# Kernel optimization log

Measured on AMD Instinct MI355X. Metric: run time of the kernel, lower is better.

Reference implementation:

```python
import jax, jax.numpy as jnp
import numpy as np

B = 4096       # batch size
DIM = 1024     # feature dim
E = 9          # 8 session experts + 1 default layer (index 8)


def setup_inputs() -> dict:
    key = jax.random.key(0)
    k_x, k_w, k_b, k_i = jax.random.split(key, 4)
    x = jax.random.normal(k_x, (B, DIM), dtype=jnp.float32)
    # Stacked nn.Linear params: W[e] has torch layout [out, in], b[e] is [out].
    # (Original init is identity+zero bias; random values exercise the same math.)
    W = jax.random.normal(k_w, (E, DIM, DIM), dtype=jnp.float32) * (DIM ** -0.5)
    b = jax.random.normal(k_b, (E, DIM), dtype=jnp.float32)
    session_idx = jax.random.randint(k_i, (B,), 0, E, dtype=jnp.int64)
    return {"x": x, "W": W, "b": b, "session_idx": session_idx}


def reference(x, W, b, session_idx):
    # Per-sample keyed linear: out[i] = x[i] @ W[session_idx[i]].T + b[session_idx[i]].
    # Dense formulation: run every expert on every sample (E small), then select.
    # y: [B, E, DIM]
    y = jnp.einsum('bd,eod->beo', x, W) + b[None, :, :]
    out = y[jnp.arange(x.shape[0]), session_idx]  # [B, DIM]
    return out
```

## Files before the change

### kernel.cpp

```cpp
#include <hip/hip_runtime.h>
#include <hip/hip_bf16.h>

#define NE 9
#define NDIM 1024
#define BM 64
#define BN 128
#define BK 64
#define NT (NDIM / BK)
#define MAX_SLOTS 80

typedef __attribute__((ext_vector_type(8))) short bf16x8;
typedef __attribute__((ext_vector_type(4))) float f32x4;

__device__ __forceinline__ unsigned pack2_bf16(float a, float b) {
    __hip_bfloat162 h = __float22bfloat162_rn(float2{a, b});
    return *reinterpret_cast<unsigned*>(&h);
}

__global__ __launch_bounds__(512)
void bucket_kernel(const int* __restrict__ sidx,
                   int* __restrict__ perm,
                   int* __restrict__ offsets,
                   int* __restrict__ slot_e,
                   int* __restrict__ slot_m0,
                   int* __restrict__ nslots,
                   int nB) {
    __shared__ int cnt[NE];
    __shared__ int cur[NE];
    int t = threadIdx.x;
    if (t < NE) cnt[t] = 0;
    __syncthreads();
    for (int i = t; i < nB; i += 512) atomicAdd(&cnt[sidx[i]], 1);
    __syncthreads();
    if (t == 0) {
        int run = 0, s = 0;
        for (int e = 0; e < NE; ++e) {
            cur[e] = run; offsets[e] = run;
            for (int m0 = 0; m0 < cnt[e]; m0 += BM) {
                slot_e[s] = e; slot_m0[s] = m0; ++s;
            }
            run += cnt[e];
        }
        offsets[NE] = run;
        *nslots = s;
    }
    __syncthreads();
    for (int i = t; i < nB; i += 512) {
        int p = atomicAdd(&cur[sidx[i]], 1);
        perm[p] = i;
    }
}

__global__ __launch_bounds__(256, 3)
void gemm_fused_kernel(const float* __restrict__ x,
                       const float* __restrict__ W,
                       const float* __restrict__ bias,
                       const int* __restrict__ perm,
                       const int* __restrict__ offsets,
                       const int* __restrict__ slot_e,
                       const int* __restrict__ slot_m0,
                       const int* __restrict__ nslots,
                       float* __restrict__ out) {
    const int b    = blockIdx.x;
    const int xcd  = b & 7;
    const int j    = b >> 3;
    const int ns   = *nslots;
    const int q    = ns >> 3, r = ns & 7;
    const int mine = q + (xcd < r ? 1 : 0);
    const int ls   = j >> 3;
    if (ls >= mine) return;
    const int slot = xcd * q + (xcd < r ? xcd : r) + ls;
    const int n    = j & 7;

    const int e   = slot_e[slot];
    const int m0  = slot_m0[slot];
    const int off = offsets[e];
    const int cnt = offsets[e + 1] - off;
    const int n0  = n * BN;

    __shared__ __align__(16) unsigned short lds[24576];

    const int t    = threadIdx.x;
    const int wave = t >> 6;
    const int lane = t & 63;
    const int fr   = lane & 15;
    const int fq   = lane >> 4;
    const int wr   = (wave >> 1) * 32;
    const int wc   = (wave & 1) * 64;
    const int xr   = fr & 7;

    const int c8 = t & 7;
    const int rg = t >> 3;
    const int wcol = (c8 ^ (rg & 7)) * 8;

    int ar0 = m0 + rg;      if (ar0 >= cnt) ar0 = cnt - 1;
    int ar1 = m0 + 32 + rg; if (ar1 >= cnt) ar1 = cnt - 1;
    const float* ap0 = x + (size_t)perm[off + ar0] * NDIM + c8 * 8;
    const float* ap1 = x + (size_t)perm[off + ar1] * NDIM + c8 * 8;
    const float* bp  = W + ((size_t)e * NDIM + n0 + rg) * NDIM + c8 * 8;

    float4 sa[4], sb[8];

#define LOADR(K0)                                                              \
    do {                                                                       \
        sa[0] = *(const float4*)(ap0 + (K0));                                  \
        sa[1] = *(const float4*)(ap0 + (K0) + 4);                              \
        sa[2] = *(const float4*)(ap1 + (K0));                                  \
        sa[3] = *(const float4*)(ap1 + (K0) + 4);                              \
        sb[0] = *(const float4*)(bp + (K0));                                   \
        sb[1] = *(const float4*)(bp + (K0) + 4);                               \
        sb[2] = *(const float4*)(bp + (size_t)32 * NDIM + (K0));               \
        sb[3] = *(const float4*)(bp + (size_t)32 * NDIM + (K0) + 4);           \
        sb[4] = *(const float4*)(bp + (size_t)64 * NDIM + (K0));               \
        sb[5] = *(const float4*)(bp + (size_t)64 * NDIM + (K0) + 4);           \
        sb[6] = *(const float4*)(bp + (size_t)96 * NDIM + (K0));               \
        sb[7] = *(const float4*)(bp + (size_t)96 * NDIM + (K0) + 4);           \
    } while (0)

#define PKW(DST, U, V)                                                         \
    do {                                                                       \
        uint4 o;                                                               \
        o.x = pack2_bf16((U).x, (U).y);                                        \
        o.y = pack2_bf16((U).z, (U).w);                                        \
        o.z = pack2_bf16((V).x, (V).y);                                        \
        o.w = pack2_bf16((V).z, (V).w);                                        \
        *reinterpret_cast<uint4*>(DST) = o;                                    \
    } while (0)

#define CVTW(BUF)                                                              \
    do {                                                                       \
        PKW(&lds[(BUF) * 4096 + rg * 64 + wcol], sa[0], sa[1]);                \
        PKW(&lds[(BUF) * 4096 + (32 + rg) * 64 + wcol], sa[2], sa[3]);         \
        PKW(&lds[8192 + (BUF) * 8192 + rg * 64 + wcol], sb[0], sb[1]);         \
        PKW(&lds[8192 + (BUF) * 8192 + (32 + rg) * 64 + wcol], sb[2], sb[3]);  \
        PKW(&lds[8192 + (BUF) * 8192 + (64 + rg) * 64 + wcol], sb[4], sb[5]);  \
        PKW(&lds[8192 + (BUF) * 8192 + (96 + rg) * 64 + wcol], sb[6], sb[7]);  \
    } while (0)

    f32x4 acc[2][4];
#pragma unroll
    for (int i = 0; i < 2; ++i)
#pragma unroll
        for (int k = 0; k < 4; ++k) acc[i][k] = (f32x4)(0.0f);

    LOADR(0);
    CVTW(0);
    LOADR(BK);
    __syncthreads();

    for (int tt = 0; tt < NT; ++tt) {
        const int curb = tt & 1;

#pragma unroll
        for (int kk = 0; kk < 2; ++kk) {
            const int cs = ((kk * 4 + fq) ^ xr) * 8;
            bf16x8 af[2], bfv[4];
#pragma unroll
            for (int mf = 0; mf < 2; ++mf)
                af[mf] = *reinterpret_cast<const bf16x8*>(
                    &lds[curb * 4096 + (wr + mf * 16 + fr) * 64 + cs]);
#pragma unroll
            for (int nf = 0; nf < 4; ++nf)
                bfv[nf] = *reinterpret_cast<const bf16x8*>(
                    &lds[8192 + curb * 8192 + (wc + nf * 16 + fr) * 64 + cs]);
            __builtin_amdgcn_s_setprio(1);
#pragma unroll
            for (int mf = 0; mf < 2; ++mf)
#pragma unroll
                for (int nf = 0; nf < 4; ++nf)
                    acc[mf][nf] = __builtin_amdgcn_mfma_f32_16x16x32_bf16(
                        af[mf], bfv[nf], acc[mf][nf], 0, 0, 0);
            __builtin_amdgcn_s_setprio(0);
        }

        if (tt + 1 < NT) {
            CVTW(curb ^ 1);
            if (tt + 2 < NT) LOADR((tt + 2) * BK);
            __syncthreads();
        }
    }
#undef LOADR
#undef PKW
#undef CVTW

    float bl[4];
#pragma unroll
    for (int nf = 0; nf < 4; ++nf)
        bl[nf] = bias[e * NDIM + n0 + wc + nf * 16 + fr];

#pragma unroll
    for (int mf = 0; mf < 2; ++mf) {
#pragma unroll
        for (int jr = 0; jr < 4; ++jr) {
            int lm = wr + mf * 16 + fq * 4 + jr;
            if (m0 + lm < cnt) {
                int grow = perm[off + m0 + lm];
                float* orow = out + (size_t)grow * NDIM;
#pragma unroll
                for (int nf = 0; nf < 4; ++nf)
                    orow[n0 + wc + nf * 16 + fr] = acc[mf][nf][jr] + bl[nf];
            }
        }
    }
}

extern "C" void kernel_launch(void* const* d_in, const int* in_sizes, int n_in,
                              void* d_out, int out_size, void* d_ws, size_t ws_size,
                              hipStream_t stream) {
    const float* x    = (const float*)d_in[0];
    const float* W    = (const float*)d_in[1];
    const float* bias = (const float*)d_in[2];
    const int*   sidx = (const int*)d_in[3];
    float*       out  = (float*)d_out;

    const int nB = in_sizes[3];

    char* wsb = (char*)d_ws;
    int* perm    = (int*)wsb;
    int* offsets = (int*)(wsb + (size_t)nB * 4);
    int* slot_e  = offsets + NE + 1;
    int* slot_m0 = slot_e + MAX_SLOTS;
    int* nslots  = slot_m0 + MAX_SLOTS;

    bucket_kernel<<<1, 512, 0, stream>>>(sidx, perm, offsets, slot_e, slot_m0,
                                         nslots, nB);

    gemm_fused_kernel<<<MAX_SLOTS * 8, 256, 0, stream>>>(
        x, W, bias, perm, offsets, slot_e, slot_m0, nslots, out);
}
```

Before: 45.19 us.

## Pre-convert x and W to bf16 and stream tiles via direct global-to-LDS loads

A prep kernel now converts all of x and W to bf16 in workspace while block 0 does the bucketing. The GEMM then loads bf16 tiles straight into LDS with global_load_lds, using a three-stage buffer and vmcnt waits instead of register staging and in-loop conversion. The aim is to halve GEMM load traffic and take conversion work off the main loop, at the cost of a full extra read and write pass over W and x. A naive fallback kernel runs if the workspace is too small.

```diff
diff --git a/kernel.cpp b/kernel.cpp
--- a/kernel.cpp
+++ b/kernel.cpp
@@ -17,50 +17,81 @@
     return *reinterpret_cast<unsigned*>(&h);
 }
 
-__global__ __launch_bounds__(512)
-void bucket_kernel(const int* __restrict__ sidx,
-                   int* __restrict__ perm,
-                   int* __restrict__ offsets,
-                   int* __restrict__ slot_e,
-                   int* __restrict__ slot_m0,
-                   int* __restrict__ nslots,
-                   int nB) {
-    __shared__ int cnt[NE];
-    __shared__ int cur[NE];
-    int t = threadIdx.x;
-    if (t < NE) cnt[t] = 0;
-    __syncthreads();
-    for (int i = t; i < nB; i += 512) atomicAdd(&cnt[sidx[i]], 1);
-    __syncthreads();
-    if (t == 0) {
-        int run = 0, s = 0;
-        for (int e = 0; e < NE; ++e) {
-            cur[e] = run; offsets[e] = run;
-            for (int m0 = 0; m0 < cnt[e]; m0 += BM) {
-                slot_e[s] = e; slot_m0[s] = m0; ++s;
+__device__ __forceinline__ void gload_lds16(const void* g, void* l) {
+    __builtin_amdgcn_global_load_lds(
+        (const __attribute__((address_space(1))) unsigned int*)g,
+        (__attribute__((address_space(3))) unsigned int*)l, 16, 0, 0);
+}
+
+__global__ __launch_bounds__(256)
+void prep_kernel(const float* __restrict__ x, const float* __restrict__ W,
+                 const int* __restrict__ sidx,
+                 unsigned short* __restrict__ xb, unsigned short* __restrict__ Wb,
+                 int* __restrict__ perm, int* __restrict__ offsets,
+                 int* __restrict__ slot_e, int* __restrict__ slot_m0,
+                 int* __restrict__ nslots, int nB) {
+    if (blockIdx.x == 0) {
+        __shared__ int cnt[NE];
+        __shared__ int cur[NE];
+        int t = threadIdx.x;
+        if (t < NE) cnt[t] = 0;
+        __syncthreads();
+        for (int i = t; i < nB; i += 256) atomicAdd(&cnt[sidx[i]], 1);
+        __syncthreads();
+        if (t == 0) {
+            int run = 0, s = 0;
+            for (int e = 0; e < NE; ++e) {
+                cur[e] = run; offsets[e] = run;
+                for (int m0 = 0; m0 < cnt[e]; m0 += BM) {
+                    slot_e[s] = e; slot_m0[s] = m0; ++s;
+                }
+                run += cnt[e];
             }
-            run += cnt[e];
-        }
-        offsets[NE] = run;
-        *nslots = s;
-    }
-    __syncthreads();
-    for (int i = t; i < nB; i += 512) {
-        int p = atomicAdd(&cur[sidx[i]], 1);
-        perm[p] = i;
-    }
-}
-
-__global__ __launch_bounds__(256, 3)
-void gemm_fused_kernel(const float* __restrict__ x,
-                       const float* __restrict__ W,
-                       const float* __restrict__ bias,
-                       const int* __restrict__ perm,
-                       const int* __restrict__ offsets,
-                       const int* __restrict__ slot_e,
-                       const int* __restrict__ slot_m0,
-                       const int* __restrict__ nslots,
-                       float* __restrict__ out) {
+            offsets[NE] = run;
+            *nslots = s;
+        }
+        __syncthreads();
+        for (int i = t; i < nB; i += 256) {
+            int p = atomicAdd(&cur[sidx[i]], 1);
+            perm[p] = i;
+        }
+    } else {
+        const int NW8 = NE * NDIM * (NDIM / 8);
+        const int NX8 = nB * (NDIM / 8);
+        const int tot = NW8 + NX8;
+        const int stride = (gridDim.x - 1) * 256;
+        for (int u = (blockIdx.x - 1) * 256 + threadIdx.x; u < tot; u += stride) {
+            const float4* src;
+            uint4* dst;
+            if (u < NW8) {
+                src = (const float4*)W + 2 * (size_t)u;
+                dst = (uint4*)Wb + u;
+            } else {
+                size_t v = (size_t)(u - NW8);
+                src = (const float4*)x + 2 * v;
+                dst = (uint4*)xb + v;
+            }
+            float4 a = src[0], c = src[1];
+            uint4 o;
+            o.x = pack2_bf16(a.x, a.y);
+            o.y = pack2_bf16(a.z, a.w);
+            o.z = pack2_bf16(c.x, c.y);
+            o.w = pack2_bf16(c.z, c.w);
+            *dst = o;
+        }
+    }
+}
+
+__global__ __launch_bounds__(256, 2)
+void gemm_bf16_kernel(const unsigned short* __restrict__ xb,
+                      const unsigned short* __restrict__ Wb,
+                      const float* __restrict__ bias,
+                      const int* __restrict__ perm,
+                      const int* __restrict__ offsets,
+                      const int* __restrict__ slot_e,
+                      const int* __restrict__ slot_m0,
+                      const int* __restrict__ nslots,
+                      float* __restrict__ out) {
     const int b    = blockIdx.x;
     const int xcd  = b & 7;
     const int j    = b >> 3;
@@ -78,7 +109,7 @@
     const int cnt = offsets[e + 1] - off;
     const int n0  = n * BN;
 
-    __shared__ __align__(16) unsigned short lds[24576];
+    __shared__ __align__(16) unsigned short lds[36864];
 
     const int t    = threadIdx.x;
     const int wave = t >> 6;
@@ -89,68 +120,47 @@
     const int wc   = (wave & 1) * 64;
     const int xr   = fr & 7;
 
-    const int c8 = t & 7;
-    const int rg = t >> 3;
-    const int wcol = (c8 ^ (rg & 7)) * 8;
-
-    int ar0 = m0 + rg;      if (ar0 >= cnt) ar0 = cnt - 1;
-    int ar1 = m0 + 32 + rg; if (ar1 >= cnt) ar1 = cnt - 1;
-    const float* ap0 = x + (size_t)perm[off + ar0] * NDIM + c8 * 8;
-    const float* ap1 = x + (size_t)perm[off + ar1] * NDIM + c8 * 8;
-    const float* bp  = W + ((size_t)e * NDIM + n0 + rg) * NDIM + c8 * 8;
-
-    float4 sa[4], sb[8];
-
-#define LOADR(K0)                                                              \
+    const int srow = t >> 3;
+    const int scol = ((t & 7) ^ (srow & 7)) * 8;
+    int lm0 = m0 + srow;      if (lm0 >= cnt) lm0 = cnt - 1;
+    int lm1 = m0 + 32 + srow; if (lm1 >= cnt) lm1 = cnt - 1;
+    const unsigned short* asrc0 = xb + (size_t)perm[off + lm0] * NDIM + scol;
+    const unsigned short* asrc1 = xb + (size_t)perm[off + lm1] * NDIM + scol;
+    const unsigned short* bsrc  = Wb + ((size_t)e * NDIM + n0 + srow) * NDIM + scol;
+
+#define STAGE(BUF, K0)                                                         \
     do {                                                                       \
-        sa[0] = *(const float4*)(ap0 + (K0));                                  \
-        sa[1] = *(const float4*)(ap0 + (K0) + 4);                              \
-        sa[2] = *(const float4*)(ap1 + (K0));                                  \
-        sa[3] = *(const float4*)(ap1 + (K0) + 4);                              \
-        sb[0] = *(const float4*)(bp + (K0));                                   \
-        sb[1] = *(const float4*)(bp + (K0) + 4);                               \
-        sb[2] = *(const float4*)(bp + (size_t)32 * NDIM + (K0));               \
-        sb[3] = *(const float4*)(bp + (size_t)32 * NDIM + (K0) + 4);           \
-        sb[4] = *(const float4*)(bp + (size_t)64 * NDIM + (K0));               \
-        sb[5] = *(const float4*)(bp + (size_t)64 * NDIM + (K0) + 4);           \
-        sb[6] = *(const float4*)(bp + (size_t)96 * NDIM + (K0));               \
-        sb[7] = *(const float4*)(bp + (size_t)96 * NDIM + (K0) + 4);           \
+        const int _ab = (BUF) * 4096;                                          \
+        const int _bb = 12288 + (BUF) * 8192;                                  \
+        gload_lds16(asrc0 + (K0), &lds[_ab + wave * 512]);                     \
+        gload_lds16(asrc1 + (K0), &lds[_ab + 2048 + wave * 512]);              \
+        _Pragma("unroll")                                                      \
+        for (int i = 0; i < 4; ++i)                                            \
+            gload_lds16(bsrc + (size_t)i * 32 * NDIM + (K0),                   \
+                        &lds[_bb + i * 2048 + wave * 512]);                    \
     } while (0)
 
-#define PKW(DST, U, V)                                                         \
-    do {                                                                       \
-        uint4 o;                                                               \
-        o.x = pack2_bf16((U).x, (U).y);                                        \
-        o.y = pack2_bf16((U).z, (U).w);                                        \
-        o.z = pack2_bf16((V).x, (V).y);                                        \
-        o.w = pack2_bf16((V).z, (V).w);                                        \
-        *reinterpret_cast<uint4*>(DST) = o;                                    \
-    } while (0)
-
-#define CVTW(BUF)                                                              \
-    do {                                                                       \
-        PKW(&lds[(BUF) * 4096 + rg * 64 + wcol], sa[0], sa[1]);                \
-        PKW(&lds[(BUF) * 4096 + (32 + rg) * 64 + wcol], sa[2], sa[3]);         \
-        PKW(&lds[8192 + (BUF) * 8192 + rg * 64 + wcol], sb[0], sb[1]);         \
-        PKW(&lds[8192 + (BUF) * 8192 + (32 + rg) * 64 + wcol], sb[2], sb[3]);  \
-        PKW(&lds[8192 + (BUF) * 8192 + (64 + rg) * 64 + wcol], sb[4], sb[5]);  \
-        PKW(&lds[8192 + (BUF) * 8192 + (96 + rg) * 64 + wcol], sb[6], sb[7]);  \
-    } while (0)
-
     f32x4 acc[2][4];
 #pragma unroll
     for (int i = 0; i < 2; ++i)
 #pragma unroll
         for (int k = 0; k < 4; ++k) acc[i][k] = (f32x4)(0.0f);
 
-    LOADR(0);
-    CVTW(0);
-    LOADR(BK);
-    __syncthreads();
-
+    STAGE(0, 0);
+    STAGE(1, BK);
+    asm volatile("s_waitcnt vmcnt(6)" ::: "memory");
+    __builtin_amdgcn_s_barrier();
+
+    int cur = 0;
+#pragma unroll
     for (int tt = 0; tt < NT; ++tt) {
-        const int curb = tt & 1;
-
+        if (tt + 2 < NT) {
+            int sb = cur + 2; if (sb >= 3) sb -= 3;
+            STAGE(sb, (tt + 2) * BK);
+        }
+
+        const int abase = cur * 4096;
+        const int bbase = 12288 + cur * 8192;
 #pragma unroll
         for (int kk = 0; kk < 2; ++kk) {
             const int cs = ((kk * 4 + fq) ^ xr) * 8;
@@ -158,30 +168,29 @@
 #pragma unroll
             for (int mf = 0; mf < 2; ++mf)
                 af[mf] = *reinterpret_cast<const bf16x8*>(
-                    &lds[curb * 4096 + (wr + mf * 16 + fr) * 64 + cs]);
+                    &lds[abase + (wr + mf * 16 + fr) * 64 + cs]);
 #pragma unroll
             for (int nf = 0; nf < 4; ++nf)
                 bfv[nf] = *reinterpret_cast<const bf16x8*>(
-                    &lds[8192 + curb * 8192 + (wc + nf * 16 + fr) * 64 + cs]);
-            __builtin_amdgcn_s_setprio(1);
+                    &lds[bbase + (wc + nf * 16 + fr) * 64 + cs]);
 #pragma unroll
             for (int mf = 0; mf < 2; ++mf)
 #pragma unroll
                 for (int nf = 0; nf < 4; ++nf)
                     acc[mf][nf] = __builtin_amdgcn_mfma_f32_16x16x32_bf16(
                         af[mf], bfv[nf], acc[mf][nf], 0, 0, 0);
-            __builtin_amdgcn_s_setprio(0);
         }
 
         if (tt + 1 < NT) {
-            CVTW(curb ^ 1);
-            if (tt + 2 < NT) LOADR((tt + 2) * BK);
-            __syncthreads();
-        }
-    }
-#undef LOADR
-#undef PKW
-#undef CVTW
+            if (tt + 2 < NT)
+                asm volatile("s_waitcnt vmcnt(6)" ::: "memory");
+            else
+                asm volatile("s_waitcnt vmcnt(0)" ::: "memory");
+            __builtin_amdgcn_s_barrier();
+        }
+        cur = (cur + 1 < 3) ? cur + 1 : 0;
+    }
+#undef STAGE
 
     float bl[4];
 #pragma unroll
@@ -202,6 +211,21 @@
             }
         }
     }
+}
+
+__global__ void naive_kernel(const float* __restrict__ x, const float* __restrict__ W,
+                             const float* __restrict__ bias,
+                             const int* __restrict__ sidx, float* __restrict__ out,
+                             int nB) {
+    int i = blockIdx.x;
+    int c = threadIdx.x + (blockIdx.y << 8);
+    if (i >= nB || c >= NDIM) return;
+    int e = sidx[i];
+    const float* w = W + ((size_t)e * NDIM + c) * NDIM;
+    const float* xr = x + (size_t)i * NDIM;
+    float s = bias[e * NDIM + c];
+    for (int k = 0; k < NDIM; ++k) s += xr[k] * w[k];
+    out[(size_t)i * NDIM + c] = s;
 }
 
 extern "C" void kernel_launch(void* const* d_in, const int* in_sizes, int n_in,
@@ -216,15 +240,31 @@
     const int nB = in_sizes[3];
 
     char* wsb = (char*)d_ws;
-    int* perm    = (int*)wsb;
-    int* offsets = (int*)(wsb + (size_t)nB * 4);
-    int* slot_e  = offsets + NE + 1;
-    int* slot_m0 = slot_e + MAX_SLOTS;
-    int* nslots  = slot_m0 + MAX_SLOTS;
-
-    bucket_kernel<<<1, 512, 0, stream>>>(sidx, perm, offsets, slot_e, slot_m0,
-                                         nslots, nB);
-
-    gemm_fused_kernel<<<MAX_SLOTS * 8, 256, 0, stream>>>(
-        x, W, bias, perm, offsets, slot_e, slot_m0, nslots, out);
-}
+    size_t p_off   = (size_t)nB * 4;
+    size_t p_slote = p_off + 64;
+    size_t p_slotm = p_slote + MAX_SLOTS * 4;
+    size_t p_nslot = p_slotm + MAX_SLOTS * 4;
+    size_t p_xb    = ((p_nslot + 4 + 511) / 512) * 512;
+    size_t p_wb    = p_xb + (size_t)nB * NDIM * 2;
+    size_t need    = p_wb + (size_t)NE * NDIM * NDIM * 2;
+
+    if (ws_size < need) {
+        dim3 g(nB, NDIM / 256);
+        naive_kernel<<<g, 256, 0, stream>>>(x, W, bias, sidx, out, nB);
+        return;
+    }
+
+    int* perm    = (int*)(wsb + 0);
+    int* offsets = (int*)(wsb + p_off);
+    int* slot_e  = (int*)(wsb + p_slote);
+    int* slot_m0 = (int*)(wsb + p_slotm);
+    int* nslots  = (int*)(wsb + p_nslot);
+    unsigned short* xb = (unsigned short*)(wsb + p_xb);
+    unsigned short* Wb = (unsigned short*)(wsb + p_wb);
+
+    prep_kernel<<<1024, 256, 0, stream>>>(x, W, sidx, xb, Wb, perm, offsets,
+                                          slot_e, slot_m0, nslots, nB);
+
+    gemm_bf16_kernel<<<MAX_SLOTS * 8, 256, 0, stream>>>(
+        xb, Wb, bias, perm, offsets, slot_e, slot_m0, nslots, out);
+}
```

Result: faster. 44.02 us (-2.6%).
